# Kernel optimization log

Measured on AMD Instinct MI355X. Metric: run time of the kernel, lower is better.

The kernel has to match this reference:

```python
import jax, jax.numpy as jnp
import numpy as np

N_NODES = 100_000
N_EDGES = 1_000_000
LATENT = 64
HID_ATOM = 256
HID_BOND = 256
RBF_DIM = 32
RBF_DMAX = 10.0
N_ATOM_TYPES = 10
N_CHARGES = 6
N_BOND_ORDERS = 5


def setup_inputs() -> dict:
    key = jax.random.key(0)
    ks = jax.random.split(key, 12)
    positions = jax.random.normal(ks[0], (N_NODES, 3), dtype=jnp.float32) * 5.0
    quantized = jax.random.normal(ks[1], (N_NODES, LATENT), dtype=jnp.float32)
    pair_indices = jax.random.randint(ks[2], (N_EDGES, 2), 0, N_NODES, dtype=jnp.int64)
    s = 0.05
    return {
        "positions": positions,
        "quantized": quantized,
        "pair_indices": pair_indices,
        "aW1": jax.random.normal(ks[3], (LATENT, HID_ATOM), jnp.float32) * s,
        "ab1": jnp.zeros((HID_ATOM,), jnp.float32),
        "aW2": jax.random.normal(ks[4], (HID_ATOM, N_ATOM_TYPES + N_CHARGES), jnp.float32) * s,
        "ab2": jnp.zeros((N_ATOM_TYPES + N_CHARGES,), jnp.float32),
        "bW1": jax.random.normal(ks[5], (LATENT + RBF_DIM, HID_BOND), jnp.float32) * s,
        "bb1": jnp.zeros((HID_BOND,), jnp.float32),
        "bW2": jax.random.normal(ks[6], (HID_BOND, N_BOND_ORDERS), jnp.float32) * s,
        "bb2": jnp.zeros((N_BOND_ORDERS,), jnp.float32),
    }


def _norm_no_nan(x, eps=1e-8):
    # L2 norm over last axis, clamped to avoid NaN gradients at 0
    return jnp.sqrt(jnp.maximum(jnp.sum(x * x, axis=-1), eps))


def _rbf(D, D_min=0.0, D_max=RBF_DMAX, D_count=RBF_DIM):
    mu = jnp.linspace(D_min, D_max, D_count, dtype=D.dtype)  # [D_count]
    sigma = (D_max - D_min) / D_count
    z = (D[..., None] - mu) / sigma
    return jnp.exp(-z * z)  # [E, D_count]


def reference(positions, quantized, pair_indices, aW1, ab1, aW2, ab2, bW1, bb1, bW2, bb2):
    src = pair_indices[:, 0]
    dst = pair_indices[:, 1]
    # pairwise distances -> RBF expansion
    x_i = positions[src]            # [E, 3]
    x_j = positions[dst]
    dists = _rbf(_norm_no_nan(x_i - x_j))  # [E, rbf_dim]
    # atom decoder (per node)
    h = jax.nn.relu(quantized @ aW1 + ab1)
    scalar_logits = h @ aW2 + ab2
    atom_type_logits = scalar_logits[:, :N_ATOM_TYPES]
    atom_charge_logits = scalar_logits[:, N_ATOM_TYPES:]
    # bond decoder (per edge): gathered latent sum concat RBF
    pair_feats = quantized[src] + quantized[dst]           # [E, latent]
    combined = jnp.concatenate([pair_feats, dists], axis=1)  # [E, latent+rbf]
    hb = jax.nn.relu(combined @ bW1 + bb1)
    bond_order_logits = hb @ bW2 + bb2
    return (atom_type_logits, atom_charge_logits, bond_order_logits)
```

## Files before the change

### kernel.cpp

```cpp
#include <hip/hip_runtime.h>
#include <hip/hip_bf16.h>

typedef __bf16 bf16x8 __attribute__((ext_vector_type(8)));
typedef __bf16 bf16x4 __attribute__((ext_vector_type(4)));
typedef float  f32x4  __attribute__((ext_vector_type(4)));

#define N_NODES 100000
#define N_EDGES 1000000
#define LATENT  64
#define HID     256
#define RBF_DIM 32
#define NTYPES  10
#define NCHG    6
#define NBOND   5

#define ATOM_TILES (N_NODES / 32)
#define ANBLK 512

#define ETILE  64
#define ETILES (N_EDGES / ETILE)
#define ENBLK  512

__global__ __launch_bounds__(256) void prep_kernel(
    const float* __restrict__ q, __bf16* __restrict__ qb)
{
    const int i = blockIdx.x * 256 + threadIdx.x;
    const float4 a = *(const float4*)(q + (size_t)i * 8);
    const float4 b = *(const float4*)(q + (size_t)i * 8 + 4);
    bf16x8 v;
    v[0] = (__bf16)a.x; v[1] = (__bf16)a.y; v[2] = (__bf16)a.z; v[3] = (__bf16)a.w;
    v[4] = (__bf16)b.x; v[5] = (__bf16)b.y; v[6] = (__bf16)b.z; v[7] = (__bf16)b.w;
    *(bf16x8*)(qb + (size_t)i * 8) = v;
}

struct __align__(16) ASmem {
    __bf16 qs[32][72];
    __bf16 hsE[32][264];
    float  red[4][2][4][64];
};

__global__ __launch_bounds__(256, 2) void atom_kernel(
    const float* __restrict__ q,   const float* __restrict__ aW1,
    const float* __restrict__ ab1, const float* __restrict__ aW2,
    const float* __restrict__ ab2, float* __restrict__ outA,
    float* __restrict__ outB)
{
    __shared__ ASmem sm;
    const int t    = threadIdx.x;
    const int w    = t >> 6;
    const int lane = t & 63;
    const int l15  = lane & 15;
    const int hi   = lane >> 4;
    const int wcol = w * 64;

    bf16x8 aw1f[2][4];
    #pragma unroll
    for (int kb = 0; kb < 2; ++kb)
        #pragma unroll
        for (int nt = 0; nt < 4; ++nt) {
            const int nn = wcol + nt * 16 + l15;
            const int k0 = kb * 32 + hi * 8;
            bf16x8 v;
            #pragma unroll
            for (int j = 0; j < 8; ++j) v[j] = (__bf16)aW1[(k0 + j) * HID + nn];
            aw1f[kb][nt] = v;
        }
    bf16x8 aw2f[2];
    #pragma unroll
    for (int kk = 0; kk < 2; ++kk) {
        const int k0 = (w * 2 + kk) * 32 + hi * 8;
        bf16x8 v;
        #pragma unroll
        for (int j = 0; j < 8; ++j) v[j] = (__bf16)aW2[(k0 + j) * 16 + l15];
        aw2f[kk] = v;
    }
    float4 b1v[4];
    #pragma unroll
    for (int nt = 0; nt < 4; ++nt)
        b1v[nt] = *(const float4*)(&ab1[wcol + nt * 16 + hi * 4]);

    const int m_st = t >> 3;
    const int p_st = t & 7;

    for (int tile = blockIdx.x; tile < ATOM_TILES; tile += ANBLK) {
        const int node0 = tile * 32;
        {
            const float* qr = q + (size_t)(node0 + m_st) * 64 + p_st * 8;
            const float4 a0 = *(const float4*)(qr);
            const float4 a1 = *(const float4*)(qr + 4);
            bf16x8 v;
            v[0] = (__bf16)a0.x; v[1] = (__bf16)a0.y; v[2] = (__bf16)a0.z; v[3] = (__bf16)a0.w;
            v[4] = (__bf16)a1.x; v[5] = (__bf16)a1.y; v[6] = (__bf16)a1.z; v[7] = (__bf16)a1.w;
            *(bf16x8*)(&sm.qs[m_st][p_st * 8]) = v;
        }
        __syncthreads();

        f32x4 acc[2][4];
        #pragma unroll
        for (int mt = 0; mt < 2; ++mt)
            #pragma unroll
            for (int nt = 0; nt < 4; ++nt) {
                f32x4 z = {0.f, 0.f, 0.f, 0.f};
                acc[mt][nt] = z;
            }
        #pragma unroll
        for (int kb = 0; kb < 2; ++kb)
            #pragma unroll
            for (int mt = 0; mt < 2; ++mt) {
                const bf16x8 bq = *(const bf16x8*)((const char*)&sm.qs[0][0]
                                   + (mt * 16 + l15) * 144 + kb * 64 + hi * 16);
                #pragma unroll
                for (int nt = 0; nt < 4; ++nt)
                    acc[mt][nt] = __builtin_amdgcn_mfma_f32_16x16x32_bf16(
                        aw1f[kb][nt], bq, acc[mt][nt], 0, 0, 0);
            }
        #pragma unroll
        for (int mt = 0; mt < 2; ++mt)
            #pragma unroll
            for (int nt = 0; nt < 4; ++nt) {
                bf16x4 hv;
                #pragma unroll
                for (int r = 0; r < 4; ++r)
                    hv[r] = (__bf16)fmaxf(acc[mt][nt][r] + ((const float*)&b1v[nt])[r], 0.f);
                *(bf16x4*)(&sm.hsE[mt * 16 + l15][wcol + nt * 16 + hi * 4]) = hv;
            }
        __syncthreads();

        f32x4 acc2[2];
        {
            f32x4 z = {0.f, 0.f, 0.f, 0.f};
            acc2[0] = z; acc2[1] = z;
        }
        #pragma unroll
        for (int mt = 0; mt < 2; ++mt)
            #pragma unroll
            for (int kk = 0; kk < 2; ++kk) {
                const int kb = w * 2 + kk;
                const bf16x8 af = *(const bf16x8*)((const char*)&sm.hsE[0][0]
                                   + (mt * 16 + l15) * 528 + kb * 64 + hi * 16);
                acc2[mt] = __builtin_amdgcn_mfma_f32_16x16x32_bf16(
                    af, aw2f[kk], acc2[mt], 0, 0, 0);
            }
        #pragma unroll
        for (int mt = 0; mt < 2; ++mt)
            #pragma unroll
            for (int r = 0; r < 4; ++r)
                sm.red[w][mt][r][lane] = acc2[mt][r];
        __syncthreads();

        {
            const int o  = t & 15;
            const int m0 = t >> 4;
            #pragma unroll
            for (int half = 0; half < 2; ++half) {
                const int m  = m0 + half * 16;
                const int mt = m >> 4, rr = m & 15;
                const int hh = rr >> 2, r = rr & 3;
                float s = ab2[o];
                #pragma unroll
                for (int ww = 0; ww < 4; ++ww) s += sm.red[ww][mt][r][hh * 16 + o];
                const int node = node0 + m;
                if (o < NTYPES) outA[node * NTYPES + o] = s;
                else            outB[node * NCHG + (o - NTYPES)] = s;
            }
        }
        __syncthreads();
    }
}

struct __align__(16) ESmem {
    __bf16 comb[ETILE][104];
    __bf16 hsE[ETILE][264];
    __bf16 w2t[16][264];
};

template<bool USEBF>
__global__ __launch_bounds__(512, 4) void edge_kernel(
    const float* __restrict__ pos, const float* __restrict__ qf,
    const __bf16* __restrict__ qb, const int* __restrict__ pair,
    const float* __restrict__ bW1, const float* __restrict__ bb1,
    const float* __restrict__ bW2, const float* __restrict__ bb2,
    float* __restrict__ outC)
{
    __shared__ ESmem sm;
    const int t    = threadIdx.x;
    const int w    = t >> 6;
    const int lane = t & 63;
    const int l15  = lane & 15;
    const int hi   = lane >> 4;
    const int wcol = w * 32;

    {
        const int o  = t >> 5;
        const int k0 = (t & 31) * 8;
        bf16x8 v;
        #pragma unroll
        for (int j = 0; j < 8; ++j)
            v[j] = (o < NBOND) ? (__bf16)bW2[(k0 + j) * NBOND + o] : (__bf16)0.f;
        *(bf16x8*)(&sm.w2t[o][k0]) = v;
    }

    bf16x8 bw1f[3][2];
    #pragma unroll
    for (int kb = 0; kb < 3; ++kb)
        #pragma unroll
        for (int nt = 0; nt < 2; ++nt) {
            const int nn = wcol + nt * 16 + l15;
            const int k0 = kb * 32 + hi * 8;
            bf16x8 v;
            #pragma unroll
            for (int j = 0; j < 8; ++j) v[j] = (__bf16)bW1[(k0 + j) * HID + nn];
            bw1f[kb][nt] = v;
        }
    float4 b1v[2];
    b1v[0] = *(const float4*)(&bb1[wcol + hi * 4]);
    b1v[1] = *(const float4*)(&bb1[wcol + 16 + hi * 4]);
    const float bb2v = (l15 < NBOND) ? bb2[l15] : 0.f;

    const int e_loc = t >> 3;
    const int p     = t & 7;

    int tile = blockIdx.x;
    int2 pA = ((const int2*)pair)[(size_t)tile * ETILE + e_loc];
    bf16x8 gs, gd;
    float4 fs0, fs1, fd0, fd1;
    float  ps0, ps1, ps2, pd0, pd1, pd2;
    if constexpr (USEBF) {
        gs = *(const bf16x8*)(qb + (size_t)pA.x * 64 + p * 8);
        gd = *(const bf16x8*)(qb + (size_t)pA.y * 64 + p * 8);
    } else {
        fs0 = *(const float4*)(qf + (size_t)pA.x * 64 + p * 8);
        fs1 = *(const float4*)(qf + (size_t)pA.x * 64 + p * 8 + 4);
        fd0 = *(const float4*)(qf + (size_t)pA.y * 64 + p * 8);
        fd1 = *(const float4*)(qf + (size_t)pA.y * 64 + p * 8 + 4);
    }
    ps0 = pos[(size_t)pA.x * 3];  ps1 = pos[(size_t)pA.x * 3 + 1];  ps2 = pos[(size_t)pA.x * 3 + 2];
    pd0 = pos[(size_t)pA.y * 3];  pd1 = pos[(size_t)pA.y * 3 + 1];  pd2 = pos[(size_t)pA.y * 3 + 2];
    {
        const int tn = tile + ENBLK;
        pA = ((const int2*)pair)[(tn < ETILES ? (size_t)tn * ETILE : 0) + e_loc];
    }
    __syncthreads();

    for (; tile < ETILES; tile += ENBLK) {
        const int e0 = tile * ETILE;

        {
            bf16x8 cv;
            if constexpr (USEBF) {
                #pragma unroll
                for (int j = 0; j < 8; ++j)
                    cv[j] = (__bf16)((float)gs[j] + (float)gd[j]);
            } else {
                cv[0] = (__bf16)(fs0.x + fd0.x); cv[1] = (__bf16)(fs0.y + fd0.y);
                cv[2] = (__bf16)(fs0.z + fd0.z); cv[3] = (__bf16)(fs0.w + fd0.w);
                cv[4] = (__bf16)(fs1.x + fd1.x); cv[5] = (__bf16)(fs1.y + fd1.y);
                cv[6] = (__bf16)(fs1.z + fd1.z); cv[7] = (__bf16)(fs1.w + fd1.w);
            }
            *(bf16x8*)(&sm.comb[e_loc][p * 8]) = cv;

            const float dx = ps0 - pd0, dy = ps1 - pd1, dz = ps2 - pd2;
            const float D  = sqrtf(fmaxf(dx * dx + dy * dy + dz * dz, 1e-8f));
            bf16x4 rv;
            #pragma unroll
            for (int j = 0; j < 4; ++j) {
                const float mu = (float)(p * 4 + j) * (10.0f / 31.0f);
                const float z  = (D - mu) * 3.2f;
                rv[j] = (__bf16)__expf(-z * z);
            }
            *(bf16x4*)(&sm.comb[e_loc][64 + p * 4]) = rv;
        }
        __syncthreads();

        {
            const int2 pN = pA;
            if constexpr (USEBF) {
                gs = *(const bf16x8*)(qb + (size_t)pN.x * 64 + p * 8);
                gd = *(const bf16x8*)(qb + (size_t)pN.y * 64 + p * 8);
            } else {
                fs0 = *(const float4*)(qf + (size_t)pN.x * 64 + p * 8);
                fs1 = *(const float4*)(qf + (size_t)pN.x * 64 + p * 8 + 4);
                fd0 = *(const float4*)(qf + (size_t)pN.y * 64 + p * 8);
                fd1 = *(const float4*)(qf + (size_t)pN.y * 64 + p * 8 + 4);
            }
            ps0 = pos[(size_t)pN.x * 3];  ps1 = pos[(size_t)pN.x * 3 + 1];  ps2 = pos[(size_t)pN.x * 3 + 2];
            pd0 = pos[(size_t)pN.y * 3];  pd1 = pos[(size_t)pN.y * 3 + 1];  pd2 = pos[(size_t)pN.y * 3 + 2];
            const int tnn = tile + 2 * ENBLK;
            pA = ((const int2*)pair)[(tnn < ETILES ? (size_t)tnn * ETILE : 0) + e_loc];
        }

        f32x4 acc[4][2];
        #pragma unroll
        for (int mt = 0; mt < 4; ++mt)
            #pragma unroll
            for (int nt = 0; nt < 2; ++nt) {
                f32x4 z = {0.f, 0.f, 0.f, 0.f};
                acc[mt][nt] = z;
            }
        #pragma unroll
        for (int kb = 0; kb < 3; ++kb)
            #pragma unroll
            for (int mt = 0; mt < 4; ++mt) {
                const bf16x8 bf = *(const bf16x8*)((const char*)&sm.comb[0][0]
                                   + (mt * 16 + l15) * 208 + kb * 64 + hi * 16);
                acc[mt][0] = __builtin_amdgcn_mfma_f32_16x16x32_bf16(
                    bw1f[kb][0], bf, acc[mt][0], 0, 0, 0);
                acc[mt][1] = __builtin_amdgcn_mfma_f32_16x16x32_bf16(
                    bw1f[kb][1], bf, acc[mt][1], 0, 0, 0);
            }
        #pragma unroll
        for (int mt = 0; mt < 4; ++mt)
            #pragma unroll
            for (int nt = 0; nt < 2; ++nt) {
                bf16x4 hv;
                #pragma unroll
                for (int r = 0; r < 4; ++r)
                    hv[r] = (__bf16)fmaxf(acc[mt][nt][r] + ((const float*)&b1v[nt])[r], 0.f);
                *(bf16x4*)((char*)&sm.hsE[0][0]
                           + (mt * 16 + l15) * 528 + (wcol + nt * 16 + hi * 4) * 2) = hv;
            }
        __syncthreads();

        if (w < 4) {
            f32x4 a2a = {0.f, 0.f, 0.f, 0.f};
            f32x4 a2b = {0.f, 0.f, 0.f, 0.f};
            #pragma unroll
            for (int kk = 0; kk < 8; kk += 2) {
                const bf16x8 af0 = *(const bf16x8*)((const char*)&sm.hsE[0][0]
                                    + (w * 16 + l15) * 528 + kk * 64 + hi * 16);
                const bf16x8 bf0 = *(const bf16x8*)((const char*)&sm.w2t[0][0]
                                    + l15 * 528 + kk * 64 + hi * 16);
                a2a = __builtin_amdgcn_mfma_f32_16x16x32_bf16(af0, bf0, a2a, 0, 0, 0);
                const bf16x8 af1 = *(const bf16x8*)((const char*)&sm.hsE[0][0]
                                    + (w * 16 + l15) * 528 + (kk + 1) * 64 + hi * 16);
                const bf16x8 bf1 = *(const bf16x8*)((const char*)&sm.w2t[0][0]
                                    + l15 * 528 + (kk + 1) * 64 + hi * 16);
                a2b = __builtin_amdgcn_mfma_f32_16x16x32_bf16(af1, bf1, a2b, 0, 0, 0);
            }
            if (l15 < NBOND) {
                #pragma unroll
                for (int r = 0; r < 4; ++r)
                    outC[(size_t)(e0 + w * 16 + hi * 4 + r) * NBOND + l15]
                        = a2a[r] + a2b[r] + bb2v;
            }
        }
    }
}

extern "C" void kernel_launch(void* const* d_in, const int* in_sizes, int n_in,
                              void* d_out, int out_size, void* d_ws, size_t ws_size,
                              hipStream_t stream)
{
    const float* pos = (const float*)d_in[0];
    const float* q   = (const float*)d_in[1];
    const int*   pair= (const int*)  d_in[2];
    const float* aW1 = (const float*)d_in[3];
    const float* ab1 = (const float*)d_in[4];
    const float* aW2 = (const float*)d_in[5];
    const float* ab2 = (const float*)d_in[6];
    const float* bW1 = (const float*)d_in[7];
    const float* bb1 = (const float*)d_in[8];
    const float* bW2 = (const float*)d_in[9];
    const float* bb2 = (const float*)d_in[10];

    float* out  = (float*)d_out;
    float* outA = out;
    float* outB = out + (size_t)N_NODES * NTYPES;
    float* outC = out + (size_t)N_NODES * (NTYPES + NCHG);

    const size_t qb_bytes = (size_t)N_NODES * LATENT * sizeof(__bf16);
    const bool use_bf = (ws_size >= qb_bytes);
    __bf16* qb = (__bf16*)d_ws;

    if (use_bf)
        hipLaunchKernelGGL(prep_kernel, dim3(N_NODES * LATENT / (256 * 8)), dim3(256),
                           0, stream, q, qb);

    hipLaunchKernelGGL(atom_kernel, dim3(ANBLK), dim3(256), 0, stream,
                       q, aW1, ab1, aW2, ab2, outA, outB);

    if (use_bf)
        hipLaunchKernelGGL(edge_kernel<true>, dim3(ENBLK), dim3(512), 0, stream,
                           pos, q, qb, pair, bW1, bb1, bW2, bb2, outC);
    else
        hipLaunchKernelGGL(edge_kernel<false>, dim3(ENBLK), dim3(512), 0, stream,
                           pos, q, qb, pair, bW1, bb1, bW2, bb2, outC);
}
```

Measured before the change: 101.9 us.

## Fuse bf16 latent conversion into atom kernel and tune edge kernel barriers

Drops the separate prep kernel and has the atom kernel write the bf16 copy of the latent while it stages it, saving one launch and one read of the fp32 latent. Biases are folded into the MFMA accumulator initial values, MFMA loops are wrapped in s_setprio raises, and gather addressing uses 32-bit unsigned math. In the edge kernel, __syncthreads is replaced by an lgkmcnt-only wait plus barrier, and one barrier is moved after the next-tile gather issue so global loads are not waited on. This carries a risk around LDS hazards if the reduced waits are insufficient.

Result: faster. 98.99 us (-2.8%).

```diff
diff --git a/kernel.cpp b/kernel.cpp
--- a/kernel.cpp
+++ b/kernel.cpp
@@ -21,29 +21,18 @@
 #define ETILES (N_EDGES / ETILE)
 #define ENBLK  512
 
-__global__ __launch_bounds__(256) void prep_kernel(
-    const float* __restrict__ q, __bf16* __restrict__ qb)
-{
-    const int i = blockIdx.x * 256 + threadIdx.x;
-    const float4 a = *(const float4*)(q + (size_t)i * 8);
-    const float4 b = *(const float4*)(q + (size_t)i * 8 + 4);
-    bf16x8 v;
-    v[0] = (__bf16)a.x; v[1] = (__bf16)a.y; v[2] = (__bf16)a.z; v[3] = (__bf16)a.w;
-    v[4] = (__bf16)b.x; v[5] = (__bf16)b.y; v[6] = (__bf16)b.z; v[7] = (__bf16)b.w;
-    *(bf16x8*)(qb + (size_t)i * 8) = v;
-}
-
 struct __align__(16) ASmem {
     __bf16 qs[32][72];
     __bf16 hsE[32][264];
     float  red[4][2][4][64];
 };
 
+template<bool EMIT_QB>
 __global__ __launch_bounds__(256, 2) void atom_kernel(
     const float* __restrict__ q,   const float* __restrict__ aW1,
     const float* __restrict__ ab1, const float* __restrict__ aW2,
     const float* __restrict__ ab2, float* __restrict__ outA,
-    float* __restrict__ outB)
+    float* __restrict__ outB,      __bf16* __restrict__ qb)
 {
     __shared__ ASmem sm;
     const int t    = threadIdx.x;
@@ -92,6 +81,8 @@
             v[0] = (__bf16)a0.x; v[1] = (__bf16)a0.y; v[2] = (__bf16)a0.z; v[3] = (__bf16)a0.w;
             v[4] = (__bf16)a1.x; v[5] = (__bf16)a1.y; v[6] = (__bf16)a1.z; v[7] = (__bf16)a1.w;
             *(bf16x8*)(&sm.qs[m_st][p_st * 8]) = v;
+            if constexpr (EMIT_QB)
+                *(bf16x8*)(qb + (size_t)(node0 + m_st) * 64 + p_st * 8) = v;
         }
         __syncthreads();
 
@@ -99,10 +90,12 @@
         #pragma unroll
         for (int mt = 0; mt < 2; ++mt)
             #pragma unroll
-            for (int nt = 0; nt < 4; ++nt) {
-                f32x4 z = {0.f, 0.f, 0.f, 0.f};
-                acc[mt][nt] = z;
-            }
+            for (int nt = 0; nt < 4; ++nt)
+                #pragma unroll
+                for (int r = 0; r < 4; ++r)
+                    acc[mt][nt][r] = ((const float*)&b1v[nt])[r];
+
+        __builtin_amdgcn_s_setprio(1);
         #pragma unroll
         for (int kb = 0; kb < 2; ++kb)
             #pragma unroll
@@ -114,6 +107,8 @@
                     acc[mt][nt] = __builtin_amdgcn_mfma_f32_16x16x32_bf16(
                         aw1f[kb][nt], bq, acc[mt][nt], 0, 0, 0);
             }
+        __builtin_amdgcn_s_setprio(0);
+
         #pragma unroll
         for (int mt = 0; mt < 2; ++mt)
             #pragma unroll
@@ -121,7 +116,7 @@
                 bf16x4 hv;
                 #pragma unroll
                 for (int r = 0; r < 4; ++r)
-                    hv[r] = (__bf16)fmaxf(acc[mt][nt][r] + ((const float*)&b1v[nt])[r], 0.f);
+                    hv[r] = (__bf16)fmaxf(acc[mt][nt][r], 0.f);
                 *(bf16x4*)(&sm.hsE[mt * 16 + l15][wcol + nt * 16 + hi * 4]) = hv;
             }
         __syncthreads();
@@ -131,6 +126,7 @@
             f32x4 z = {0.f, 0.f, 0.f, 0.f};
             acc2[0] = z; acc2[1] = z;
         }
+        __builtin_amdgcn_s_setprio(1);
         #pragma unroll
         for (int mt = 0; mt < 2; ++mt)
             #pragma unroll
@@ -141,6 +137,7 @@
                 acc2[mt] = __builtin_amdgcn_mfma_f32_16x16x32_bf16(
                     af, aw2f[kk], acc2[mt], 0, 0, 0);
             }
+        __builtin_amdgcn_s_setprio(0);
         #pragma unroll
         for (int mt = 0; mt < 2; ++mt)
             #pragma unroll
@@ -173,6 +170,11 @@
     __bf16 hsE[ETILE][264];
     __bf16 w2t[16][264];
 };
+
+__device__ __forceinline__ void bar_lgkm() {
+    asm volatile("s_waitcnt lgkmcnt(0)" ::: "memory");
+    __builtin_amdgcn_s_barrier();
+}
 
 template<bool USEBF>
 __global__ __launch_bounds__(512, 4) void edge_kernel(
@@ -226,16 +228,16 @@
     float4 fs0, fs1, fd0, fd1;
     float  ps0, ps1, ps2, pd0, pd1, pd2;
     if constexpr (USEBF) {
-        gs = *(const bf16x8*)(qb + (size_t)pA.x * 64 + p * 8);
-        gd = *(const bf16x8*)(qb + (size_t)pA.y * 64 + p * 8);
+        gs = *(const bf16x8*)(qb + ((unsigned)pA.x * 64u + (unsigned)(p * 8)));
+        gd = *(const bf16x8*)(qb + ((unsigned)pA.y * 64u + (unsigned)(p * 8)));
     } else {
-        fs0 = *(const float4*)(qf + (size_t)pA.x * 64 + p * 8);
-        fs1 = *(const float4*)(qf + (size_t)pA.x * 64 + p * 8 + 4);
-        fd0 = *(const float4*)(qf + (size_t)pA.y * 64 + p * 8);
-        fd1 = *(const float4*)(qf + (size_t)pA.y * 64 + p * 8 + 4);
-    }
-    ps0 = pos[(size_t)pA.x * 3];  ps1 = pos[(size_t)pA.x * 3 + 1];  ps2 = pos[(size_t)pA.x * 3 + 2];
-    pd0 = pos[(size_t)pA.y * 3];  pd1 = pos[(size_t)pA.y * 3 + 1];  pd2 = pos[(size_t)pA.y * 3 + 2];
+        fs0 = *(const float4*)(qf + ((unsigned)pA.x * 64u + (unsigned)(p * 8)));
+        fs1 = *(const float4*)(qf + ((unsigned)pA.x * 64u + (unsigned)(p * 8) + 4u));
+        fd0 = *(const float4*)(qf + ((unsigned)pA.y * 64u + (unsigned)(p * 8)));
+        fd1 = *(const float4*)(qf + ((unsigned)pA.y * 64u + (unsigned)(p * 8) + 4u));
+    }
+    ps0 = pos[(unsigned)pA.x * 3u];  ps1 = pos[(unsigned)pA.x * 3u + 1u];  ps2 = pos[(unsigned)pA.x * 3u + 2u];
+    pd0 = pos[(unsigned)pA.y * 3u];  pd1 = pos[(unsigned)pA.y * 3u + 1u];  pd2 = pos[(unsigned)pA.y * 3u + 2u];
     {
         const int tn = tile + ENBLK;
         pA = ((const int2*)pair)[(tn < ETILES ? (size_t)tn * ETILE : 0) + e_loc];
@@ -270,33 +272,35 @@
             }
             *(bf16x4*)(&sm.comb[e_loc][64 + p * 4]) = rv;
         }
-        __syncthreads();
 
         {
             const int2 pN = pA;
             if constexpr (USEBF) {
-                gs = *(const bf16x8*)(qb + (size_t)pN.x * 64 + p * 8);
-                gd = *(const bf16x8*)(qb + (size_t)pN.y * 64 + p * 8);
+                gs = *(const bf16x8*)(qb + ((unsigned)pN.x * 64u + (unsigned)(p * 8)));
+                gd = *(const bf16x8*)(qb + ((unsigned)pN.y * 64u + (unsigned)(p * 8)));
             } else {
-                fs0 = *(const float4*)(qf + (size_t)pN.x * 64 + p * 8);
-                fs1 = *(const float4*)(qf + (size_t)pN.x * 64 + p * 8 + 4);
-                fd0 = *(const float4*)(qf + (size_t)pN.y * 64 + p * 8);
-                fd1 = *(const float4*)(qf + (size_t)pN.y * 64 + p * 8 + 4);
-            }
-            ps0 = pos[(size_t)pN.x * 3];  ps1 = pos[(size_t)pN.x * 3 + 1];  ps2 = pos[(size_t)pN.x * 3 + 2];
-            pd0 = pos[(size_t)pN.y * 3];  pd1 = pos[(size_t)pN.y * 3 + 1];  pd2 = pos[(size_t)pN.y * 3 + 2];
+                fs0 = *(const float4*)(qf + ((unsigned)pN.x * 64u + (unsigned)(p * 8)));
+                fs1 = *(const float4*)(qf + ((unsigned)pN.x * 64u + (unsigned)(p * 8) + 4u));
+                fd0 = *(const float4*)(qf + ((unsigned)pN.y * 64u + (unsigned)(p * 8)));
+                fd1 = *(const float4*)(qf + ((unsigned)pN.y * 64u + (unsigned)(p * 8) + 4u));
+            }
+            ps0 = pos[(unsigned)pN.x * 3u];  ps1 = pos[(unsigned)pN.x * 3u + 1u];  ps2 = pos[(unsigned)pN.x * 3u + 2u];
+            pd0 = pos[(unsigned)pN.y * 3u];  pd1 = pos[(unsigned)pN.y * 3u + 1u];  pd2 = pos[(unsigned)pN.y * 3u + 2u];
             const int tnn = tile + 2 * ENBLK;
             pA = ((const int2*)pair)[(tnn < ETILES ? (size_t)tnn * ETILE : 0) + e_loc];
         }
+        bar_lgkm();
 
         f32x4 acc[4][2];
         #pragma unroll
         for (int mt = 0; mt < 4; ++mt)
             #pragma unroll
-            for (int nt = 0; nt < 2; ++nt) {
-                f32x4 z = {0.f, 0.f, 0.f, 0.f};
-                acc[mt][nt] = z;
-            }
+            for (int nt = 0; nt < 2; ++nt)
+                #pragma unroll
+                for (int r = 0; r < 4; ++r)
+                    acc[mt][nt][r] = ((const float*)&b1v[nt])[r];
+
+        __builtin_amdgcn_s_setprio(1);
         #pragma unroll
         for (int kb = 0; kb < 3; ++kb)
             #pragma unroll
@@ -308,6 +312,8 @@
                 acc[mt][1] = __builtin_amdgcn_mfma_f32_16x16x32_bf16(
                     bw1f[kb][1], bf, acc[mt][1], 0, 0, 0);
             }
+        __builtin_amdgcn_s_setprio(0);
+
         #pragma unroll
         for (int mt = 0; mt < 4; ++mt)
             #pragma unroll
@@ -315,15 +321,17 @@
                 bf16x4 hv;
                 #pragma unroll
                 for (int r = 0; r < 4; ++r)
-                    hv[r] = (__bf16)fmaxf(acc[mt][nt][r] + ((const float*)&b1v[nt])[r], 0.f);
+                    hv[r] = (__bf16)fmaxf(acc[mt][nt][r], 0.f);
                 *(bf16x4*)((char*)&sm.hsE[0][0]
                            + (mt * 16 + l15) * 528 + (wcol + nt * 16 + hi * 4) * 2) = hv;
             }
-        __syncthreads();
+        bar_lgkm();
 
         if (w < 4) {
-            f32x4 a2a = {0.f, 0.f, 0.f, 0.f};
-            f32x4 a2b = {0.f, 0.f, 0.f, 0.f};
+            f32x4 a2a, a2b;
+            #pragma unroll
+            for (int r = 0; r < 4; ++r) { a2a[r] = bb2v; a2b[r] = 0.f; }
+            __builtin_amdgcn_s_setprio(1);
             #pragma unroll
             for (int kk = 0; kk < 8; kk += 2) {
                 const bf16x8 af0 = *(const bf16x8*)((const char*)&sm.hsE[0][0]
@@ -337,11 +345,12 @@
                                     + l15 * 528 + (kk + 1) * 64 + hi * 16);
                 a2b = __builtin_amdgcn_mfma_f32_16x16x32_bf16(af1, bf1, a2b, 0, 0, 0);
             }
+            __builtin_amdgcn_s_setprio(0);
             if (l15 < NBOND) {
                 #pragma unroll
                 for (int r = 0; r < 4; ++r)
                     outC[(size_t)(e0 + w * 16 + hi * 4 + r) * NBOND + l15]
-                        = a2a[r] + a2b[r] + bb2v;
+                        = a2a[r] + a2b[r];
             }
         }
     }
@@ -373,11 +382,11 @@
     __bf16* qb = (__bf16*)d_ws;
 
     if (use_bf)
-        hipLaunchKernelGGL(prep_kernel, dim3(N_NODES * LATENT / (256 * 8)), dim3(256),
-                           0, stream, q, qb);
-
-    hipLaunchKernelGGL(atom_kernel, dim3(ANBLK), dim3(256), 0, stream,
-                       q, aW1, ab1, aW2, ab2, outA, outB);
+        hipLaunchKernelGGL(atom_kernel<true>, dim3(ANBLK), dim3(256), 0, stream,
+                           q, aW1, ab1, aW2, ab2, outA, outB, qb);
+    else
+        hipLaunchKernelGGL(atom_kernel<false>, dim3(ANBLK), dim3(256), 0, stream,
+                           q, aW1, ab1, aW2, ab2, outA, outB, qb);
 
     if (use_bf)
         hipLaunchKernelGGL(edge_kernel<true>, dim3(ENBLK), dim3(512), 0, stream,
```
